# Performance work log

Hardware: AMD Instinct MI355X
Metric: run time of the kernel (lower is better)

The kernel has to match this reference:

```python
import jax, jax.numpy as jnp
import numpy as np

B, H, S, E = 16384, 16, 1, 64
N_OTHERS = 4


def setup_inputs() -> dict:
    key = jax.random.key(0)
    ks = jax.random.split(key, N_OTHERS + 2)
    inp = {f"others_{i}": jax.random.normal(ks[i], (B, H, S, E), dtype=jnp.float32)
           for i in range(N_OTHERS)}
    inp["main"] = jax.random.normal(ks[N_OTHERS], (B, H, S, E), dtype=jnp.float32)
    inp["W"] = jax.random.normal(ks[N_OTHERS + 1], (E, E), dtype=jnp.float32) * (1.0 / np.sqrt(E))
    return inp


def reference(others_0, others_1, others_2, others_3, main, W):
    # mean over the 'others' modalities: (B, H, 1, E)
    mean = (others_0 + others_1 + others_2 + others_3) / 4.0
    m = jnp.squeeze(mean, 2)        # (B, H, E)
    main_sq = jnp.squeeze(main, 2)  # (B, H, E)
    # bilinear score: mean @ W @ main^T -> (B, H, H)
    score = jnp.einsum('bhe,ef,bgf->bhg', m, W, main_sq)
    attn = jax.nn.softmax(score, axis=-1)      # (B, H, H)
    context = jnp.einsum('bhg,bge->bhe', attn, main_sq)  # (B, H, E)
    return context, attn
```

## Files before the change

kernel.cpp:

```cpp
#include <hip/hip_runtime.h>

#define NBATCH 16384
#define H 16
#define E 64

#define LGKM0 do { asm volatile("s_waitcnt lgkmcnt(0)" ::: "memory"); \
                   __builtin_amdgcn_sched_barrier(0); } while (0)

__global__ __launch_bounds__(64, 3) void ovo_kernel(
    const float* __restrict__ o0, const float* __restrict__ o1,
    const float* __restrict__ o2, const float* __restrict__ o3,
    const float* __restrict__ mn, const float* __restrict__ W,
    float* __restrict__ ctx_out, float* __restrict__ attn_out)
{
    __shared__ float sA[H * 68];
    __shared__ float sMain[H * 68];

    const int l = threadIdx.x;
    const size_t base = (size_t)blockIdx.x * (H * E);

    float4 ra[4], rb[4], rc[4], rd[4], rv[4];
#pragma unroll
    for (int k = 0; k < 4; ++k) {
        const int off = k * 256 + l * 4;
        ra[k] = *(const float4*)(o0 + base + off);
        rb[k] = *(const float4*)(o1 + base + off);
        rc[k] = *(const float4*)(o2 + base + off);
        rd[k] = *(const float4*)(o3 + base + off);
        rv[k] = *(const float4*)(mn + base + off);
    }

#pragma unroll
    for (int k = 0; k < 4; ++k) {
        const int flat = k * 256 + l * 4;
        const int h = flat >> 6, e = flat & 63;
        float4 m4;
        m4.x = (ra[k].x + rb[k].x + rc[k].x + rd[k].x) * 0.25f;
        m4.y = (ra[k].y + rb[k].y + rc[k].y + rd[k].y) * 0.25f;
        m4.z = (ra[k].z + rb[k].z + rc[k].z + rd[k].z) * 0.25f;
        m4.w = (ra[k].w + rb[k].w + rc[k].w + rd[k].w) * 0.25f;
        *(float4*)&sA[h * 68 + e] = m4;
        *(float4*)&sMain[h * 68 + e] = rv[k];
    }
    LGKM0;

    {
        const int ht = l >> 4, ft = l & 15;
        const int h0 = ht * 4, f0 = ft * 4;
        float acc[4][4] = {{0.f}};
#pragma unroll
        for (int e0 = 0; e0 < 64; e0 += 4) {
            float4 mrow[4], wrow[4];
#pragma unroll
            for (int i = 0; i < 4; ++i) mrow[i] = *(const float4*)&sA[(h0 + i) * 68 + e0];
#pragma unroll
            for (int j = 0; j < 4; ++j) wrow[j] = *(const float4*)&W[(e0 + j) * 64 + f0];
#pragma unroll
            for (int i = 0; i < 4; ++i) {
                const float* mr = (const float*)&mrow[i];
#pragma unroll
                for (int ee = 0; ee < 4; ++ee) {
                    const float* wr = (const float*)&wrow[ee];
#pragma unroll
                    for (int j = 0; j < 4; ++j)
                        acc[i][j] = fmaf(mr[ee], wr[j], acc[i][j]);
                }
            }
        }
        LGKM0;
#pragma unroll
        for (int i = 0; i < 4; ++i)
            *(float4*)&sA[(h0 + i) * 68 + f0] =
                make_float4(acc[i][0], acc[i][1], acc[i][2], acc[i][3]);
    }
    LGKM0;

    const int hp = l >> 2, gp = l & 3;
    const int g0 = gp * 4;
    float sc[4] = {0.f, 0.f, 0.f, 0.f};
#pragma unroll
    for (int f0 = 0; f0 < 64; f0 += 4) {
        float4 a0 = *(const float4*)&sA[hp * 68 + f0];
        const float* pa = (const float*)&a0;
        float4 b[4];
#pragma unroll
        for (int j = 0; j < 4; ++j)
            b[j] = *(const float4*)&sMain[(g0 + j) * 68 + f0];
#pragma unroll
        for (int j = 0; j < 4; ++j) {
            const float* pb = (const float*)&b[j];
#pragma unroll
            for (int q = 0; q < 4; ++q)
                sc[j] = fmaf(pa[q], pb[q], sc[j]);
        }
    }
    LGKM0;

    {
        float mx = fmaxf(fmaxf(sc[0], sc[1]), fmaxf(sc[2], sc[3]));
        mx = fmaxf(mx, __shfl_xor(mx, 1));
        mx = fmaxf(mx, __shfl_xor(mx, 2));
        float e0 = __expf(sc[0] - mx), e1 = __expf(sc[1] - mx);
        float e2 = __expf(sc[2] - mx), e3 = __expf(sc[3] - mx);
        float sum = (e0 + e1) + (e2 + e3);
        sum += __shfl_xor(sum, 1);
        sum += __shfl_xor(sum, 2);
        const float inv = 1.0f / sum;
        float4 a4 = make_float4(e0 * inv, e1 * inv, e2 * inv, e3 * inv);
        *(float4*)(attn_out + (size_t)blockIdx.x * (H * H) + l * 4) = a4;
        const float* pa4 = (const float*)&a4;
#pragma unroll
        for (int j = 0; j < 4; ++j)
            sA[(g0 + j) * 20 + hp] = pa4[j];
    }
    LGKM0;

    {
        const int ht = l >> 4, et = l & 15;
        const int h0 = ht * 4, e0c = et * 4;
        float acc[4][4] = {{0.f}};
#pragma unroll
        for (int g = 0; g < 16; ++g) {
            float4 bv = *(const float4*)&sMain[g * 68 + e0c];
            float4 av = *(const float4*)&sA[g * 20 + h0];
            const float* pb = (const float*)&bv;
            const float* pa = (const float*)&av;
#pragma unroll
            for (int i = 0; i < 4; ++i)
#pragma unroll
                for (int j = 0; j < 4; ++j)
                    acc[i][j] = fmaf(pa[i], pb[j], acc[i][j]);
        }
        float* cp = ctx_out + base;
#pragma unroll
        for (int i = 0; i < 4; ++i)
            *(float4*)(cp + (h0 + i) * 64 + e0c) =
                make_float4(acc[i][0], acc[i][1], acc[i][2], acc[i][3]);
    }
}

extern "C" void kernel_launch(void* const* d_in, const int* in_sizes, int n_in,
                              void* d_out, int out_size, void* d_ws, size_t ws_size,
                              hipStream_t stream) {
    const float* o0 = (const float*)d_in[0];
    const float* o1 = (const float*)d_in[1];
    const float* o2 = (const float*)d_in[2];
    const float* o3 = (const float*)d_in[3];
    const float* mn = (const float*)d_in[4];
    const float* W  = (const float*)d_in[5];
    float* ctx  = (float*)d_out;
    float* attn = ctx + (size_t)NBATCH * H * E;
    hipLaunchKernelGGL(ovo_kernel, dim3(NBATCH), dim3(64), 0, stream,
                       o0, o1, o2, o3, mn, W, ctx, attn);
}
```

Measured before the change: 91.69 us.

## Stage W in shared memory and loop each wave over several batches

Each block now has four waves. The block loads the 64x64 W matrix into LDS once, and each wave then processes four batch elements in a loop with its own private LDS tiles. Before, every 64-thread block read W from global memory (through cache) for each batch. The change is meant to remove those repeated global W loads and cut block launch overhead. The cost is a larger LDS footprint per block (16KB for W plus 34KB of tiles), which may limit occupancy, and a serialized per-wave loop with no prefetch of the next batch.

```diff
diff --git a/kernel.cpp b/kernel.cpp
--- a/kernel.cpp
+++ b/kernel.cpp
@@ -3,139 +3,160 @@
 #define NBATCH 16384
 #define H 16
 #define E 64
+#define NB 4
+#define NWAVE 4
+#define NBLK (NBATCH / (NB * NWAVE))
 
 #define LGKM0 do { asm volatile("s_waitcnt lgkmcnt(0)" ::: "memory"); \
                    __builtin_amdgcn_sched_barrier(0); } while (0)
 
-__global__ __launch_bounds__(64, 3) void ovo_kernel(
+__global__ __launch_bounds__(256, 3) void ovo_kernel(
     const float* __restrict__ o0, const float* __restrict__ o1,
     const float* __restrict__ o2, const float* __restrict__ o3,
     const float* __restrict__ mn, const float* __restrict__ W,
     float* __restrict__ ctx_out, float* __restrict__ attn_out)
 {
-    __shared__ float sA[H * 68];
-    __shared__ float sMain[H * 68];
+    __shared__ float sW[E * E];
+    __shared__ float sT[NWAVE][2][H * 68];
 
-    const int l = threadIdx.x;
-    const size_t base = (size_t)blockIdx.x * (H * E);
-
-    float4 ra[4], rb[4], rc[4], rd[4], rv[4];
-#pragma unroll
-    for (int k = 0; k < 4; ++k) {
-        const int off = k * 256 + l * 4;
-        ra[k] = *(const float4*)(o0 + base + off);
-        rb[k] = *(const float4*)(o1 + base + off);
-        rc[k] = *(const float4*)(o2 + base + off);
-        rd[k] = *(const float4*)(o3 + base + off);
-        rv[k] = *(const float4*)(mn + base + off);
-    }
+    const int tid = threadIdx.x;
+    const int l   = tid & 63;
+    const int wv  = tid >> 6;
 
 #pragma unroll
-    for (int k = 0; k < 4; ++k) {
-        const int flat = k * 256 + l * 4;
-        const int h = flat >> 6, e = flat & 63;
-        float4 m4;
-        m4.x = (ra[k].x + rb[k].x + rc[k].x + rd[k].x) * 0.25f;
-        m4.y = (ra[k].y + rb[k].y + rc[k].y + rd[k].y) * 0.25f;
-        m4.z = (ra[k].z + rb[k].z + rc[k].z + rd[k].z) * 0.25f;
-        m4.w = (ra[k].w + rb[k].w + rc[k].w + rd[k].w) * 0.25f;
-        *(float4*)&sA[h * 68 + e] = m4;
-        *(float4*)&sMain[h * 68 + e] = rv[k];
+    for (int c = 0; c < 4; ++c) {
+        const int idx = c * 1024 + tid * 4;
+        *(float4*)&sW[idx] = *(const float4*)&W[idx];
     }
-    LGKM0;
+    __syncthreads();
 
-    {
-        const int ht = l >> 4, ft = l & 15;
-        const int h0 = ht * 4, f0 = ft * 4;
-        float acc[4][4] = {{0.f}};
+    float* const sA    = &sT[wv][0][0];
+    float* const sMain = &sT[wv][1][0];
+
+#pragma unroll 1
+    for (int it = 0; it < NB; ++it) {
+        const int batch = it * (NBLK * NWAVE) + blockIdx.x * NWAVE + wv;
+        const size_t base = (size_t)batch * (H * E);
+
+        float4 ra[4], rb[4], rc[4], rd[4], rv[4];
 #pragma unroll
-        for (int e0 = 0; e0 < 64; e0 += 4) {
-            float4 mrow[4], wrow[4];
+        for (int k = 0; k < 4; ++k) {
+            const int off = k * 256 + l * 4;
+            ra[k] = *(const float4*)(o0 + base + off);
+            rb[k] = *(const float4*)(o1 + base + off);
+            rc[k] = *(const float4*)(o2 + base + off);
+            rd[k] = *(const float4*)(o3 + base + off);
+            rv[k] = *(const float4*)(mn + base + off);
+        }
+
 #pragma unroll
-            for (int i = 0; i < 4; ++i) mrow[i] = *(const float4*)&sA[(h0 + i) * 68 + e0];
+        for (int k = 0; k < 4; ++k) {
+            const int flat = k * 256 + l * 4;
+            const int h = flat >> 6, e = flat & 63;
+            float4 m4;
+            m4.x = (ra[k].x + rb[k].x + rc[k].x + rd[k].x) * 0.25f;
+            m4.y = (ra[k].y + rb[k].y + rc[k].y + rd[k].y) * 0.25f;
+            m4.z = (ra[k].z + rb[k].z + rc[k].z + rd[k].z) * 0.25f;
+            m4.w = (ra[k].w + rb[k].w + rc[k].w + rd[k].w) * 0.25f;
+            *(float4*)&sA[h * 68 + e] = m4;
+            *(float4*)&sMain[h * 68 + e] = rv[k];
+        }
+        LGKM0;
+
+        {
+            const int ht = l >> 4, ft = l & 15;
+            const int h0 = ht * 4, f0 = ft * 4;
+            float acc[4][4] = {{0.f}};
 #pragma unroll
-            for (int j = 0; j < 4; ++j) wrow[j] = *(const float4*)&W[(e0 + j) * 64 + f0];
+            for (int e0 = 0; e0 < 64; e0 += 4) {
+                float4 mrow[4], wrow[4];
 #pragma unroll
-            for (int i = 0; i < 4; ++i) {
-                const float* mr = (const float*)&mrow[i];
+                for (int i = 0; i < 4; ++i) mrow[i] = *(const float4*)&sA[(h0 + i) * 68 + e0];
 #pragma unroll
-                for (int ee = 0; ee < 4; ++ee) {
-                    const float* wr = (const float*)&wrow[ee];
+                for (int j = 0; j < 4; ++j) wrow[j] = *(const float4*)&sW[(e0 + j) * 64 + f0];
 #pragma unroll
-                    for (int j = 0; j < 4; ++j)
-                        acc[i][j] = fmaf(mr[ee], wr[j], acc[i][j]);
+                for (int i = 0; i < 4; ++i) {
+                    const float* mr = (const float*)&mrow[i];
+#pragma unroll
+                    for (int ee = 0; ee < 4; ++ee) {
+                        const float* wr = (const float*)&wrow[ee];
+#pragma unroll
+                        for (int j = 0; j < 4; ++j)
+                            acc[i][j] = fmaf(mr[ee], wr[j], acc[i][j]);
+                    }
                 }
+            }
+            LGKM0;
+#pragma unroll
+            for (int i = 0; i < 4; ++i)
+                *(float4*)&sA[(h0 + i) * 68 + f0] =
+                    make_float4(acc[i][0], acc[i][1], acc[i][2], acc[i][3]);
+        }
+        LGKM0;
+
+        const int hp = l >> 2, gp = l & 3;
+        const int g0 = gp * 4;
+        float scr[4] = {0.f, 0.f, 0.f, 0.f};
+#pragma unroll
+        for (int f0 = 0; f0 < 64; f0 += 4) {
+            float4 a0 = *(const float4*)&sA[hp * 68 + f0];
+            const float* pa = (const float*)&a0;
+            float4 b[4];
+#pragma unroll
+            for (int j = 0; j < 4; ++j)
+                b[j] = *(const float4*)&sMain[(g0 + j) * 68 + f0];
+#pragma unroll
+            for (int j = 0; j < 4; ++j) {
+                const float* pb = (const float*)&b[j];
+#pragma unroll
+                for (int q = 0; q < 4; ++q)
+                    scr[j] = fmaf(pa[q], pb[q], scr[j]);
             }
         }
         LGKM0;
+
+        {
+            float mx = fmaxf(fmaxf(scr[0], scr[1]), fmaxf(scr[2], scr[3]));
+            mx = fmaxf(mx, __shfl_xor(mx, 1));
+            mx = fmaxf(mx, __shfl_xor(mx, 2));
+            float e0 = __expf(scr[0] - mx), e1 = __expf(scr[1] - mx);
+            float e2 = __expf(scr[2] - mx), e3 = __expf(scr[3] - mx);
+            float sum = (e0 + e1) + (e2 + e3);
+            sum += __shfl_xor(sum, 1);
+            sum += __shfl_xor(sum, 2);
+            const float inv = 1.0f / sum;
+            float4 a4 = make_float4(e0 * inv, e1 * inv, e2 * inv, e3 * inv);
+            *(float4*)(attn_out + (size_t)batch * (H * H) + l * 4) = a4;
+            const float* pa4 = (const float*)&a4;
 #pragma unroll
-        for (int i = 0; i < 4; ++i)
-            *(float4*)&sA[(h0 + i) * 68 + f0] =
-                make_float4(acc[i][0], acc[i][1], acc[i][2], acc[i][3]);
-    }
-    LGKM0;
+            for (int j = 0; j < 4; ++j)
+                sA[(g0 + j) * 20 + hp] = pa4[j];
+        }
+        LGKM0;
 
-    const int hp = l >> 2, gp = l & 3;
-    const int g0 = gp * 4;
-    float sc[4] = {0.f, 0.f, 0.f, 0.f};
+        {
+            const int ht = l >> 4, et = l & 15;
+            const int h0 = ht * 4, e0c = et * 4;
+            float acc[4][4] = {{0.f}};
 #pragma unroll
-    for (int f0 = 0; f0 < 64; f0 += 4) {
-        float4 a0 = *(const float4*)&sA[hp * 68 + f0];
-        const float* pa = (const float*)&a0;
-        float4 b[4];
+            for (int g = 0; g < 16; ++g) {
+                float4 bv = *(const float4*)&sMain[g * 68 + e0c];
+                float4 av = *(const float4*)&sA[g * 20 + h0];
+                const float* pb = (const float*)&bv;
+                const float* pa = (const float*)&av;
 #pragma unroll
-        for (int j = 0; j < 4; ++j)
-            b[j] = *(const float4*)&sMain[(g0 + j) * 68 + f0];
+                for (int i = 0; i < 4; ++i)
 #pragma unroll
-        for (int j = 0; j < 4; ++j) {
-            const float* pb = (const float*)&b[j];
-#pragma unroll
-            for (int q = 0; q < 4; ++q)
-                sc[j] = fmaf(pa[q], pb[q], sc[j]);
-        }
-    }
-    LGKM0;
-
-    {
-        float mx = fmaxf(fmaxf(sc[0], sc[1]), fmaxf(sc[2], sc[3]));
-        mx = fmaxf(mx, __shfl_xor(mx, 1));
-        mx = fmaxf(mx, __shfl_xor(mx, 2));
-        float e0 = __expf(sc[0] - mx), e1 = __expf(sc[1] - mx);
-        float e2 = __expf(sc[2] - mx), e3 = __expf(sc[3] - mx);
-        float sum = (e0 + e1) + (e2 + e3);
-        sum += __shfl_xor(sum, 1);
-        sum += __shfl_xor(sum, 2);
-        const float inv = 1.0f / sum;
-        float4 a4 = make_float4(e0 * inv, e1 * inv, e2 * inv, e3 * inv);
-        *(float4*)(attn_out + (size_t)blockIdx.x * (H * H) + l * 4) = a4;
-        const float* pa4 = (const float*)&a4;
-#pragma unroll
-        for (int j = 0; j < 4; ++j)
-            sA[(g0 + j) * 20 + hp] = pa4[j];
-    }
-    LGKM0;
-
-    {
-        const int ht = l >> 4, et = l & 15;
-        const int h0 = ht * 4, e0c = et * 4;
-        float acc[4][4] = {{0.f}};
-#pragma unroll
-        for (int g = 0; g < 16; ++g) {
-            float4 bv = *(const float4*)&sMain[g * 68 + e0c];
-            float4 av = *(const float4*)&sA[g * 20 + h0];
-            const float* pb = (const float*)&bv;
-            const float* pa = (const float*)&av;
+                    for (int j = 0; j < 4; ++j)
+                        acc[i][j] = fmaf(pa[i], pb[j], acc[i][j]);
+            }
+            float* cp = ctx_out + base;
 #pragma unroll
             for (int i = 0; i < 4; ++i)
-#pragma unroll
-                for (int j = 0; j < 4; ++j)
-                    acc[i][j] = fmaf(pa[i], pb[j], acc[i][j]);
+                *(float4*)(cp + (h0 + i) * 64 + e0c) =
+                    make_float4(acc[i][0], acc[i][1], acc[i][2], acc[i][3]);
         }
-        float* cp = ctx_out + base;
-#pragma unroll
-        for (int i = 0; i < 4; ++i)
-            *(float4*)(cp + (h0 + i) * 64 + e0c) =
-                make_float4(acc[i][0], acc[i][1], acc[i][2], acc[i][3]);
+        LGKM0;
     }
 }
 
@@ -150,6 +171,6 @@
     const float* W  = (const float*)d_in[5];
     float* ctx  = (float*)d_out;
     float* attn = ctx + (size_t)NBATCH * H * E;
-    hipLaunchKernelGGL(ovo_kernel, dim3(NBATCH), dim3(64), 0, stream,
+    hipLaunchKernelGGL(ovo_kernel, dim3(NBLK), dim3(NWAVE * 64), 0, stream,
                        o0, o1, o2, o3, mn, W, ctx, attn);
 }
```

New measurement: 91.70 us. Within noise of the previous version (+0.0%).
